# Kernel optimization log

Hardware: AMD Instinct MI355X
Metric: run time of the kernel (lower is better)

## Reference

```python
import jax, jax.numpy as jnp
import numpy as np

WIN = 8
NUM_LAYERS = 2
HID = 512
GROUPS = 4
GH = 2 * HID // GROUPS  # 256


def _shuffle(y):
    # torch Shuffle: transpose(-1,-2).contiguous().view(original_shape)
    return jnp.swapaxes(y, -1, -2).reshape(y.shape)


def _gru_cell(xt, h, w_ih, w_hh, b_ih, b_hh):
    # torch.nn.GRUCell math; gate order r, z, n
    gi = xt @ w_ih.T + b_ih  # [B, 3H]
    gh = h @ w_hh.T + b_hh   # [B, 3H]
    i_r, i_z, i_n = jnp.split(gi, 3, axis=1)
    h_r, h_z, h_n = jnp.split(gh, 3, axis=1)
    r = jax.nn.sigmoid(i_r + h_r)
    z = jax.nn.sigmoid(i_z + h_z)
    n = jnp.tanh(i_n + r * h_n)
    return (1.0 - z) * n + z * h


def _sort_attn(h, a1, a2, a3, a4):
    B, H = h.shape
    s = jnp.sort(h, axis=1)                 # stable sort along features
    se = jnp.stack((h, s), axis=1)          # [B, 2, H]
    y = se @ a1.T                           # Linear(H, H) -> [B, 2, H]
    y = y.reshape(B, GROUPS, GH)            # Flatten + Unflatten
    y = _shuffle(y)
    y = y @ a2.T                            # Linear(GH, GH)
    y = _shuffle(y)
    y = jax.nn.relu(y @ a3.T)               # Linear(GH, GH) + ReLU
    y = y.reshape(B, GROUPS * GH)           # [B, 2H]
    scores = jax.nn.sigmoid(y @ a4.T)       # Linear(2H, H) -> [B, H]
    return h * scores


def setup_inputs() -> dict:
    key = jax.random.key(0)
    ks = jax.random.split(key, 10)
    B, L, C = 64, 4096, 64
    sc = 0.05
    inp = {
        "x": jax.random.normal(ks[0], (B, L, C), dtype=jnp.float32),
        "hidden0": jnp.zeros((NUM_LAYERS, 1, HID), dtype=jnp.float32),
        "w_ih": jax.random.normal(ks[1], (NUM_LAYERS, 3 * HID, HID), dtype=jnp.float32) * sc,
        "w_hh": jax.random.normal(ks[2], (NUM_LAYERS, 3 * HID, HID), dtype=jnp.float32) * sc,
        "b_ih": jax.random.normal(ks[3], (NUM_LAYERS, 3 * HID), dtype=jnp.float32) * sc,
        "b_hh": jax.random.normal(ks[4], (NUM_LAYERS, 3 * HID), dtype=jnp.float32) * sc,
        "a1": jax.random.normal(ks[5], (NUM_LAYERS, HID, HID), dtype=jnp.float32) * sc,
        "a2": jax.random.normal(ks[6], (NUM_LAYERS, GH, GH), dtype=jnp.float32) * sc,
        "a3": jax.random.normal(ks[7], (NUM_LAYERS, GH, GH), dtype=jnp.float32) * sc,
        "a4": jax.random.normal(ks[8], (NUM_LAYERS, HID, 2 * HID), dtype=jnp.float32) * sc,
    }
    return inp


def reference(x, hidden0, w_ih, w_hh, b_ih, b_hh, a1, a2, a3, a4):
    B, L, C = x.shape
    xp = x.reshape(B, L // WIN, WIN * C)
    xs = jnp.swapaxes(xp, 0, 1)                       # [T, B, D]
    h0 = jnp.broadcast_to(hidden0, (NUM_LAYERS, B, HID))

    def step(hid, xt):
        inp = xt
        new = []
        for l in range(NUM_LAYERS):
            h = _gru_cell(inp, hid[l], w_ih[l], w_hh[l], b_ih[l], b_hh[l])
            h = _sort_attn(h, a1[l], a2[l], a3[l], a4[l])
            new.append(h)
            inp = h
        return jnp.stack(new, axis=0), inp

    _, outs = jax.lax.scan(step, h0, xs)              # outs: [T, B, H]
    return jnp.swapaxes(outs, 0, 1)                   # [B, T, H]
```

## Files before the change

### kernel.cpp

```cpp
#include <hip/hip_runtime.h>

#define SCOPE_AGENT __HIP_MEMORY_SCOPE_AGENT

#define OFF_HS    0
#define OFF_HP    65536
#define OFF_SG    131072
#define OFF_U     196608
#define OFF_CTR   327680
#define OFF_T1    393216
#define OFF_M     2490368
#define OFF_GIX   4587520
#define OFF_XT    4587520
#define WS_GIX    54919168
#define WS_XT     21364736

typedef float f32x4 __attribute__((ext_vector_type(4)));

__device__ __forceinline__ float sigm(float x) { return 1.f / (1.f + expf(-x)); }

__device__ __forceinline__ float ld_sc1(const float* p) {
    return __hip_atomic_load(p, __ATOMIC_RELAXED, SCOPE_AGENT);
}
__device__ __forceinline__ void st_sc1(float* p, float v) {
    __hip_atomic_store(p, v, __ATOMIC_RELAXED, SCOPE_AGENT);
}
__device__ __forceinline__ void st2(float* p, float a, float b) {
    unsigned long long v = ((unsigned long long)__float_as_uint(b) << 32) |
                           (unsigned long long)__float_as_uint(a);
    __hip_atomic_store((unsigned long long*)p, v, __ATOMIC_RELAXED, SCOPE_AGENT);
}

__device__ __forceinline__ void ld4b8(const float* base, f32x4* v) {
    const float* b2 = base + 1024;
    asm volatile(
        "global_load_dwordx4 %0, %8, off sc1\n\t"
        "global_load_dwordx4 %1, %8, off offset:1024 sc1\n\t"
        "global_load_dwordx4 %2, %8, off offset:2048 sc1\n\t"
        "global_load_dwordx4 %3, %8, off offset:3072 sc1\n\t"
        "global_load_dwordx4 %4, %9, off sc1\n\t"
        "global_load_dwordx4 %5, %9, off offset:1024 sc1\n\t"
        "global_load_dwordx4 %6, %9, off offset:2048 sc1\n\t"
        "global_load_dwordx4 %7, %9, off offset:3072 sc1\n\t"
        "s_waitcnt vmcnt(0)"
        : "=&v"(v[0]), "=&v"(v[1]), "=&v"(v[2]), "=&v"(v[3]),
          "=&v"(v[4]), "=&v"(v[5]), "=&v"(v[6]), "=&v"(v[7])
        : "v"(base), "v"(b2)
        : "memory");
}

__device__ __forceinline__ void ld4b8x2(const float* baseA, const float* baseB,
                                        f32x4* va, f32x4* vb) {
    const float* a2 = baseA + 1024;
    const float* b2 = baseB + 1024;
    asm volatile(
        "global_load_dwordx4 %0, %16, off sc1\n\t"
        "global_load_dwordx4 %1, %16, off offset:1024 sc1\n\t"
        "global_load_dwordx4 %2, %16, off offset:2048 sc1\n\t"
        "global_load_dwordx4 %3, %16, off offset:3072 sc1\n\t"
        "global_load_dwordx4 %4, %17, off sc1\n\t"
        "global_load_dwordx4 %5, %17, off offset:1024 sc1\n\t"
        "global_load_dwordx4 %6, %17, off offset:2048 sc1\n\t"
        "global_load_dwordx4 %7, %17, off offset:3072 sc1\n\t"
        "global_load_dwordx4 %8, %18, off sc1\n\t"
        "global_load_dwordx4 %9, %18, off offset:1024 sc1\n\t"
        "global_load_dwordx4 %10, %18, off offset:2048 sc1\n\t"
        "global_load_dwordx4 %11, %18, off offset:3072 sc1\n\t"
        "global_load_dwordx4 %12, %19, off sc1\n\t"
        "global_load_dwordx4 %13, %19, off offset:1024 sc1\n\t"
        "global_load_dwordx4 %14, %19, off offset:2048 sc1\n\t"
        "global_load_dwordx4 %15, %19, off offset:3072 sc1\n\t"
        "s_waitcnt vmcnt(0)"
        : "=&v"(va[0]), "=&v"(va[1]), "=&v"(va[2]), "=&v"(va[3]),
          "=&v"(va[4]), "=&v"(va[5]), "=&v"(va[6]), "=&v"(va[7]),
          "=&v"(vb[0]), "=&v"(vb[1]), "=&v"(vb[2]), "=&v"(vb[3]),
          "=&v"(vb[4]), "=&v"(vb[5]), "=&v"(vb[6]), "=&v"(vb[7])
        : "v"(baseA), "v"(a2), "v"(baseB), "v"(b2)
        : "memory");
}

__device__ __forceinline__ void gbar(unsigned* flags, unsigned g) {
    __syncthreads();
    const int tid = threadIdx.x;
    if (tid == 0)
        __hip_atomic_store(&flags[blockIdx.x << 5], g, __ATOMIC_RELAXED, SCOPE_AGENT);
    if (tid < 256) {
        while (__hip_atomic_load(&flags[tid << 5], __ATOMIC_RELAXED, SCOPE_AGENT) < g)
            __builtin_amdgcn_s_sleep(1);
    }
    __syncthreads();
}

__global__ void k_init(const float* __restrict__ h0, float* __restrict__ ws) {
    int idx = blockIdx.x * blockDim.x + threadIdx.x;
    int l = idx >> 15, k = (idx & 32767) >> 6, lane = idx & 63;
    ws[OFF_HS + (l << 15) + ((k >> 2) << 8) + (lane << 2) + (k & 3)] = h0[(l << 9) + k];
    if (idx < 8704) ((unsigned*)(ws + OFF_CTR))[idx] = 0u;
}

__global__ void k_gix(const float* __restrict__ x, const float* __restrict__ wih,
                      float* __restrict__ gix) {
    __shared__ float xs[128][65];
    __shared__ float ww[32][129];
    int t = blockIdx.x, rb = blockIdx.y * 32;
    int tid = threadIdx.x;
    int rw = tid >> 6, b = tid & 63;
    float acc[8] = {0.f, 0.f, 0.f, 0.f, 0.f, 0.f, 0.f, 0.f};
    for (int kc = 0; kc < 4; kc++) {
        __syncthreads();
        for (int i = tid; i < 8192; i += 256) {
            int k = i & 127, b2 = i >> 7;
            xs[k][b2] = x[(size_t)b2 * 262144 + (size_t)t * 512 + kc * 128 + k];
        }
        for (int i = tid; i < 4096; i += 256) {
            int r = i >> 7, k = i & 127;
            ww[r][k] = wih[(size_t)(rb + r) * 512 + kc * 128 + k];
        }
        __syncthreads();
        for (int k = 0; k < 128; k++) {
            float xv = xs[k][b];
#pragma unroll
            for (int rr = 0; rr < 8; rr++)
                acc[rr] = fmaf(ww[rw * 8 + rr][k], xv, acc[rr]);
        }
    }
#pragma unroll
    for (int rr = 0; rr < 8; rr++) {
        int rg = rb + rw * 8 + rr;
        int g = rg >> 9, j = rg & 511;
        gix[((size_t)((size_t)t * 512 + j) * 3 + g) * 64 + b] = acc[rr];
    }
}

__global__ void k_xtk(const float* __restrict__ x, float* __restrict__ xT) {
    __shared__ float tile[64][65];
    int t = blockIdx.x >> 3, kc = blockIdx.x & 7;
    int k = threadIdx.x & 63, b0 = threadIdx.x >> 6;
    for (int i = 0; i < 16; i++) {
        int b = i * 4 + b0;
        tile[k][b] = x[(size_t)b * 262144 + (size_t)t * 512 + kc * 64 + k];
    }
    __syncthreads();
    int b2 = threadIdx.x & 63, k0 = threadIdx.x >> 6;
    for (int i = 0; i < 16; i++) {
        int k2 = kc * 64 + i * 4 + k0;
        xT[(size_t)t * 32768 + ((k2 >> 2) << 8) + (b2 << 2) + (k2 & 3)] = tile[i * 4 + k0][b2];
    }
}

__global__ void k_t1(const float* __restrict__ a1, const float* __restrict__ a2,
                     float* __restrict__ T1) {
    int l = blockIdx.x >> 10, c = blockIdx.x & 1023;
    int g = c >> 8, jj = c & 255;
    __shared__ float sA2[256];
    sA2[threadIdx.x] = a2[l * 65536 + jj * 256 + threadIdx.x];
    __syncthreads();
    const float* A1l = a1 + l * 262144;
    for (int colq = 0; colq < 4; colq++) {
        int col = colq * 256 + threadIdx.x;
        int half = col >> 9, cm = col & 511;
        float acc = 0.f;
#pragma unroll 4
        for (int q = 0; q < 64; q++) {
            int a0 = 2 * half;
            int j0 = g * 64 + q;
            acc = fmaf(sA2[4 * q + a0],     A1l[j0 * 512 + cm], acc);
            acc = fmaf(sA2[4 * q + a0 + 1], A1l[(j0 + 256) * 512 + cm], acc);
        }
        T1[((size_t)(l << 10) + c) * 1024 + col] = acc;
    }
}

__global__ void k_m(const float* __restrict__ a3, const float* __restrict__ T1,
                    float* __restrict__ M) {
    int l = blockIdx.x >> 10, c = blockIdx.x & 1023;
    int g = c >> 8, jj = c & 255;
    __shared__ float sA3[256];
    sA3[threadIdx.x] = a3[l * 65536 + jj * 256 + threadIdx.x];
    __syncthreads();
    const float* T1l = T1 + ((size_t)l << 20);
    for (int colq = 0; colq < 4; colq++) {
        int col = colq * 256 + threadIdx.x;
        float acc = 0.f;
#pragma unroll 4
        for (int m = 0; m < 256; m++) {
            int p = ((m & 3) << 8) + (g << 6) + (m >> 2);
            acc = fmaf(sA3[m], T1l[p * 1024 + col], acc);
        }
        M[((size_t)(l << 10) + c) * 1024 + col] = acc;
    }
}

__global__ void __launch_bounds__(1024, 4)
persist(const float* __restrict__ x, const float* __restrict__ xT,
        const float* __restrict__ gix, int has_xt, int has_gix,
        const float* __restrict__ wih, const float* __restrict__ whh,
        const float* __restrict__ bih, const float* __restrict__ bhh,
        const float* __restrict__ Mc, const float* __restrict__ a4,
        float* __restrict__ ws, float* __restrict__ out) {
    __shared__ float wA[2][2][6][512];
    __shared__ float wM[2][4][1024];
    __shared__ float wD[2][2][1024];
    __shared__ float red2[12][16][64];
    __shared__ float bb[2][2][4];
    __shared__ float sH[2][2][64];

    const int tid = threadIdx.x, w = tid >> 6, lane = tid & 63, bid = blockIdx.x;

    for (int i = tid; i < 12288; i += 1024) {
        int l = i / 6144, r = i % 6144, f = r / 3072, r2 = r % 3072, d = r2 / 512, k = r2 & 511;
        int gate = d >> 1, side = d & 1;
        int j = 2 * bid + f;
        const float* src = side ? whh : wih;
        wA[l][f][d][k] = src[l * 786432 + (gate * 512 + j) * 512 + k];
    }
    for (int i = tid; i < 8192; i += 1024) {
        int l = i >> 12, r = (i >> 10) & 3, col = i & 1023;
        wM[l][r][col] = Mc[((size_t)(l << 10) + 4 * bid + r) * 1024 + col];
    }
    for (int i = tid; i < 4096; i += 1024) {
        int l = i >> 11, f = (i >> 10) & 1, k = i & 1023;
        wD[l][f][k] = a4[l * 524288 + (2 * bid + f) * 1024 + k];
    }
    if (tid < 16) {
        int l = tid / 8, f = (tid / 4) & 1, g = tid & 3;
        int j = 2 * bid + f;
        float v;
        if (g == 0)      v = bih[l * 1536 + j] + bhh[l * 1536 + j];
        else if (g == 1) v = bih[l * 1536 + 512 + j] + bhh[l * 1536 + 512 + j];
        else if (g == 2) v = bih[l * 1536 + 1024 + j];
        else             v = bhh[l * 1536 + 1024 + j];
        bb[l][f][g] = v;
    }
    __syncthreads();

    float* hsG = ws + OFF_HS;
    float* hPg = ws + OFF_HP;
    float* sGg = ws + OFF_SG;
    float* uG  = ws + OFF_U;
    unsigned* flags = (unsigned*)(ws + OFF_CTR);
    unsigned bgen = 0;

    auto stageA = [&](int l, int t) {
        float hprev = 0.f;
        if (w < 2) {
            int j = 2 * bid + w;
            hprev = ld_sc1(&hsG[(l << 15) + ((j >> 2) << 8) + (lane << 2) + (j & 3)]);
        }
        const float* hb = hsG + (l << 15);
        float* hPl = hPg + (l << 15);
        int k0 = w * 32;
        const int koff = ((k0 >> 2) << 8) + (lane << 2);
        if (l == 0 && has_gix) {
            float acc[6] = {0.f, 0.f, 0.f, 0.f, 0.f, 0.f};
            f32x4 hv[8];
            ld4b8(hb + koff, hv);
#pragma unroll
            for (int m = 0; m < 8; m++) {
#pragma unroll
                for (int q = 0; q < 4; q++) {
                    int k = k0 + 4 * m + q;
                    float h = hv[m][q];
#pragma unroll
                    for (int f = 0; f < 2; f++) {
                        acc[f * 3 + 0] = fmaf(wA[0][f][1][k], h, acc[f * 3 + 0]);
                        acc[f * 3 + 1] = fmaf(wA[0][f][3][k], h, acc[f * 3 + 1]);
                        acc[f * 3 + 2] = fmaf(wA[0][f][5][k], h, acc[f * 3 + 2]);
                    }
                }
            }
#pragma unroll
            for (int u = 0; u < 6; u++) red2[u][w][lane] = acc[u];
            __syncthreads();
            if (w < 2) {
                int f = w, j = 2 * bid + f;
                float s0 = 0, s1 = 0, s2 = 0;
#pragma unroll
                for (int i = 0; i < 16; i++) {
                    s0 += red2[f * 3 + 0][i][lane];
                    s1 += red2[f * 3 + 1][i][lane];
                    s2 += red2[f * 3 + 2][i][lane];
                }
                const float* gx = gix + ((size_t)((size_t)t * 512 + j) * 3) * 64;
                float r = sigm(gx[lane] + s0 + bb[0][f][0]);
                float z = sigm(gx[64 + lane] + s1 + bb[0][f][1]);
                float n = tanhf(gx[128 + lane] + bb[0][f][2] + r * (s2 + bb[0][f][3]));
                float hp = (1.f - z) * n + z * hprev;
                sH[0][f][lane] = hp;
                st_sc1(&hPl[((j >> 2) << 8) + (lane << 2) + (j & 3)], hp);
            }
        } else {
            float acc[12];
#pragma unroll
            for (int u = 0; u < 12; u++) acc[u] = 0.f;
            f32x4 iv[8], hv[8];
            if (l == 1) {
                ld4b8x2(hsG + koff, hb + koff, iv, hv);
            } else if (has_xt) {
                ld4b8x2(xT + (size_t)t * 32768 + koff, hb + koff, iv, hv);
            } else {
#pragma unroll
                for (int m = 0; m < 8; m++)
#pragma unroll
                    for (int q = 0; q < 4; q++)
                        iv[m][q] = x[(size_t)lane * 262144 + (size_t)t * 512 + k0 + 4 * m + q];
                ld4b8(hb + koff, hv);
            }
#pragma unroll
            for (int m = 0; m < 8; m++) {
#pragma unroll
                for (int q = 0; q < 4; q++) {
                    int k = k0 + 4 * m + q;
                    float ivq = iv[m][q];
#pragma unroll
                    for (int f = 0; f < 2; f++) {
                        acc[f * 6 + 0] = fmaf(wA[l][f][0][k], ivq, acc[f * 6 + 0]);
                        acc[f * 6 + 2] = fmaf(wA[l][f][2][k], ivq, acc[f * 6 + 2]);
                        acc[f * 6 + 4] = fmaf(wA[l][f][4][k], ivq, acc[f * 6 + 4]);
                    }
                }
            }
#pragma unroll
            for (int m = 0; m < 8; m++) {
#pragma unroll
                for (int q = 0; q < 4; q++) {
                    int k = k0 + 4 * m + q;
                    float h = hv[m][q];
#pragma unroll
                    for (int f = 0; f < 2; f++) {
                        acc[f * 6 + 1] = fmaf(wA[l][f][1][k], h, acc[f * 6 + 1]);
                        acc[f * 6 + 3] = fmaf(wA[l][f][3][k], h, acc[f * 6 + 3]);
                        acc[f * 6 + 5] = fmaf(wA[l][f][5][k], h, acc[f * 6 + 5]);
                    }
                }
            }
#pragma unroll
            for (int u = 0; u < 12; u++) red2[u][w][lane] = acc[u];
            __syncthreads();
            if (w < 2) {
                int f = w, j = 2 * bid + f;
                float g0 = 0, g1 = 0, g2 = 0, g3 = 0, g4 = 0, g5 = 0;
#pragma unroll
                for (int i = 0; i < 16; i++) {
                    g0 += red2[f * 6 + 0][i][lane]; g1 += red2[f * 6 + 1][i][lane];
                    g2 += red2[f * 6 + 2][i][lane]; g3 += red2[f * 6 + 3][i][lane];
                    g4 += red2[f * 6 + 4][i][lane]; g5 += red2[f * 6 + 5][i][lane];
                }
                float r = sigm(g0 + g1 + bb[l][f][0]);
                float z = sigm(g2 + g3 + bb[l][f][1]);
                float n = tanhf(g4 + bb[l][f][2] + r * (g5 + bb[l][f][3]));
                float hp = (1.f - z) * n + z * hprev;
                sH[l][f][lane] = hp;
                st_sc1(&hPl[((j >> 2) << 8) + (lane << 2) + (j & 3)], hp);
            }
        }
    };

    auto stageB = [&](int l, float* accB) {
        int j0 = 2 * bid, j1 = j0 + 1;
        float v0 = sH[l][0][lane], v1 = sH[l][1][lane];
        const float* hPl = hPg + (l << 15);
        float* sGl = sGg + (l << 15);
        int k0 = w * 32, cnt0 = 0, cnt1 = 0;
        accB[0] = accB[1] = accB[2] = accB[3] = 0.f;
        f32x4 hv[8];
        ld4b8(hPl + ((k0 >> 2) << 8) + (lane << 2), hv);
#pragma unroll
        for (int m = 0; m < 8; m++) {
#pragma unroll
            for (int q = 0; q < 4; q++) {
                int k = k0 + 4 * m + q;
                float h = hv[m][q];
                cnt0 += (h < v0 || (h == v0 && k < j0)) ? 1 : 0;
                cnt1 += (h < v1 || (h == v1 && k < j1)) ? 1 : 0;
#pragma unroll
                for (int r = 0; r < 4; r++)
                    accB[r] = fmaf(wM[l][r][k], h, accB[r]);
            }
        }
        red2[0][w][lane] = (float)cnt0;
        red2[1][w][lane] = (float)cnt1;
        __syncthreads();
        if (w < 2) {
            int rk = 0;
#pragma unroll
            for (int i = 0; i < 16; i++) rk += (int)red2[w][i][lane];
            st_sc1(&sGl[((rk >> 2) << 8) + (lane << 2) + (rk & 3)], sH[l][w][lane]);
        }
    };

    auto stageC = [&](int l, const float* accB) {
        float acc[4] = {accB[0], accB[1], accB[2], accB[3]};
        int s0 = w * 32;
        const float* sGl = sGg + (l << 15);
        f32x4 sv[8];
        ld4b8(sGl + ((s0 >> 2) << 8) + (lane << 2), sv);
#pragma unroll
        for (int m = 0; m < 8; m++) {
#pragma unroll
            for (int q = 0; q < 4; q++) {
                int sp = s0 + 4 * m + q;
                float vv = sv[m][q];
#pragma unroll
                for (int r = 0; r < 4; r++)
                    acc[r] = fmaf(wM[l][r][512 + sp], vv, acc[r]);
            }
        }
#pragma unroll
        for (int r = 0; r < 4; r++) red2[r][w][lane] = acc[r];
        __syncthreads();
        if (w < 2) {
            float sa = 0.f, sb = 0.f;
#pragma unroll
            for (int i = 0; i < 16; i++) {
                sa += red2[2 * w + 0][i][lane];
                sb += red2[2 * w + 1][i][lane];
            }
            st2(&uG[(l << 16) + (bid << 8) + (lane << 2) + (w << 1)],
                fmaxf(sa, 0.f), fmaxf(sb, 0.f));
        }
    };

    auto stageD = [&](int l, int t) {
        float a0 = 0.f, a1v = 0.f;
        int k0 = w * 64;
        const float* uL = uG + (l << 16);
        f32x4 uv[8], uw[8];
        ld4b8x2(uL + ((k0 >> 2) << 8) + (lane << 2),
                uL + (((k0 >> 2) + 8) << 8) + (lane << 2), uv, uw);
#pragma unroll
        for (int m = 0; m < 8; m++)
#pragma unroll
            for (int q = 0; q < 4; q++) {
                int k = k0 + 4 * m + q;
                a0 = fmaf(wD[l][0][k], uv[m][q], a0);
                a1v = fmaf(wD[l][1][k], uv[m][q], a1v);
            }
#pragma unroll
        for (int m = 0; m < 8; m++)
#pragma unroll
            for (int q = 0; q < 4; q++) {
                int k = k0 + 32 + 4 * m + q;
                a0 = fmaf(wD[l][0][k], uw[m][q], a0);
                a1v = fmaf(wD[l][1][k], uw[m][q], a1v);
            }
        red2[0][w][lane] = a0;
        red2[1][w][lane] = a1v;
        __syncthreads();
        if (w < 2) {
            float s = 0.f;
#pragma unroll
            for (int i = 0; i < 16; i++) s += red2[w][i][lane];
            float hnew = sH[l][w][lane] * sigm(s);
            int j = 2 * bid + w;
            st_sc1(&hsG[(l << 15) + ((j >> 2) << 8) + (lane << 2) + (j & 3)], hnew);
            if (l == 1)
                out[(size_t)lane * 262144 + (size_t)t * 512 + j] = hnew;
        }
    };

    float accB0[4], accB1[4];

    for (int t = 0; t <= 512; t++) {
        const int t0 = t, t1 = t - 1;
        const bool do0 = (t0 < 512), do1 = (t1 >= 0);

        if (do0) stageA(0, t0);
        if (do1) { __syncthreads(); stageA(1, t1); }
        gbar(flags, ++bgen);

        if (do0) stageB(0, accB0);
        if (do1) { __syncthreads(); stageB(1, accB1); }
        gbar(flags, ++bgen);

        if (do0) stageC(0, accB0);
        if (do1) { __syncthreads(); stageC(1, accB1); }
        gbar(flags, ++bgen);

        if (do0) stageD(0, t0);
        if (do1) { __syncthreads(); stageD(1, t1); }
        gbar(flags, ++bgen);
    }
}

extern "C" void kernel_launch(void* const* d_in, const int* in_sizes, int n_in,
                              void* d_out, int out_size, void* d_ws, size_t ws_size,
                              hipStream_t stream) {
    const float* x   = (const float*)d_in[0];
    const float* h0  = (const float*)d_in[1];
    const float* wih = (const float*)d_in[2];
    const float* whh = (const float*)d_in[3];
    const float* bih = (const float*)d_in[4];
    const float* bhh = (const float*)d_in[5];
    const float* a1  = (const float*)d_in[6];
    const float* a2  = (const float*)d_in[7];
    const float* a3  = (const float*)d_in[8];
    const float* a4  = (const float*)d_in[9];
    float* ws  = (float*)d_ws;
    float* out = (float*)d_out;

    int has_gix = (ws_size >= (size_t)WS_GIX * 4) ? 1 : 0;
    int has_xt  = (!has_gix && ws_size >= (size_t)WS_XT * 4) ? 1 : 0;
    float* T1p = ws + OFF_T1;
    float* Mp  = ws + OFF_M;
    const float* gixp = ws + OFF_GIX;
    const float* xTp  = ws + OFF_XT;

    hipLaunchKernelGGL(k_init, dim3(256), dim3(256), 0, stream, h0, ws);
    if (has_gix)
        hipLaunchKernelGGL(k_gix, dim3(512, 48), dim3(256), 0, stream, x, wih, ws + OFF_GIX);
    else if (has_xt)
        hipLaunchKernelGGL(k_xtk, dim3(4096), dim3(256), 0, stream, x, ws + OFF_XT);
    hipLaunchKernelGGL(k_t1, dim3(2048), dim3(256), 0, stream, a1, a2, T1p);
    hipLaunchKernelGGL(k_m, dim3(2048), dim3(256), 0, stream, a3, T1p, Mp);

    void* args[] = {(void*)&x, (void*)&xTp, (void*)&gixp, (void*)&has_xt, (void*)&has_gix,
                    (void*)&wih, (void*)&whh, (void*)&bih, (void*)&bhh,
                    (void*)&Mp, (void*)&a4, (void*)&ws, (void*)&out};
    hipLaunchCooperativeKernel((void*)persist, dim3(256), dim3(1024), args, 0, stream);
}
```

Measured before the change: 43.46 ms.

## Merge layer-0 and layer-1 stage work per phase to halve block-level syncs

```diff
diff --git a/kernel.cpp b/kernel.cpp
--- a/kernel.cpp
+++ b/kernel.cpp
@@ -200,7 +200,7 @@
     __shared__ float wA[2][2][6][512];
     __shared__ float wM[2][4][1024];
     __shared__ float wD[2][2][1024];
-    __shared__ float red2[12][16][64];
+    __shared__ float red2[14][16][64];
     __shared__ float bb[2][2][4];
     __shared__ float sH[2][2][64];
 
@@ -240,7 +240,7 @@
     unsigned* flags = (unsigned*)(ws + OFF_CTR);
     unsigned bgen = 0;
 
-    auto stageA = [&](int l, int t) {
+    auto stageA_legacy = [&](int l, int t) {
         float hprev = 0.f;
         if (w < 2) {
             int j = 2 * bid + w;
@@ -250,28 +250,134 @@
         float* hPl = hPg + (l << 15);
         int k0 = w * 32;
         const int koff = ((k0 >> 2) << 8) + (lane << 2);
-        if (l == 0 && has_gix) {
-            float acc[6] = {0.f, 0.f, 0.f, 0.f, 0.f, 0.f};
-            f32x4 hv[8];
+        float acc[12];
+#pragma unroll
+        for (int u = 0; u < 12; u++) acc[u] = 0.f;
+        f32x4 iv[8], hv[8];
+        if (l == 1) {
+            ld4b8x2(hsG + koff, hb + koff, iv, hv);
+        } else if (has_xt) {
+            ld4b8x2(xT + (size_t)t * 32768 + koff, hb + koff, iv, hv);
+        } else {
+#pragma unroll
+            for (int m = 0; m < 8; m++)
+#pragma unroll
+                for (int q = 0; q < 4; q++)
+                    iv[m][q] = x[(size_t)lane * 262144 + (size_t)t * 512 + k0 + 4 * m + q];
             ld4b8(hb + koff, hv);
-#pragma unroll
-            for (int m = 0; m < 8; m++) {
-#pragma unroll
-                for (int q = 0; q < 4; q++) {
-                    int k = k0 + 4 * m + q;
-                    float h = hv[m][q];
-#pragma unroll
-                    for (int f = 0; f < 2; f++) {
-                        acc[f * 3 + 0] = fmaf(wA[0][f][1][k], h, acc[f * 3 + 0]);
-                        acc[f * 3 + 1] = fmaf(wA[0][f][3][k], h, acc[f * 3 + 1]);
-                        acc[f * 3 + 2] = fmaf(wA[0][f][5][k], h, acc[f * 3 + 2]);
-                    }
-                }
-            }
-#pragma unroll
-            for (int u = 0; u < 6; u++) red2[u][w][lane] = acc[u];
+        }
+#pragma unroll
+        for (int m = 0; m < 8; m++) {
+#pragma unroll
+            for (int q = 0; q < 4; q++) {
+                int k = k0 + 4 * m + q;
+                float ivq = iv[m][q], h = hv[m][q];
+#pragma unroll
+                for (int f = 0; f < 2; f++) {
+                    acc[f * 6 + 0] = fmaf(wA[l][f][0][k], ivq, acc[f * 6 + 0]);
+                    acc[f * 6 + 1] = fmaf(wA[l][f][1][k], h, acc[f * 6 + 1]);
+                    acc[f * 6 + 2] = fmaf(wA[l][f][2][k], ivq, acc[f * 6 + 2]);
+                    acc[f * 6 + 3] = fmaf(wA[l][f][3][k], h, acc[f * 6 + 3]);
+                    acc[f * 6 + 4] = fmaf(wA[l][f][4][k], ivq, acc[f * 6 + 4]);
+                    acc[f * 6 + 5] = fmaf(wA[l][f][5][k], h, acc[f * 6 + 5]);
+                }
+            }
+        }
+#pragma unroll
+        for (int u = 0; u < 12; u++) red2[u][w][lane] = acc[u];
+        __syncthreads();
+        if (w < 2) {
+            int f = w, j = 2 * bid + f;
+            float g0 = 0, g1 = 0, g2 = 0, g3 = 0, g4 = 0, g5 = 0;
+#pragma unroll
+            for (int i = 0; i < 16; i++) {
+                g0 += red2[f * 6 + 0][i][lane]; g1 += red2[f * 6 + 1][i][lane];
+                g2 += red2[f * 6 + 2][i][lane]; g3 += red2[f * 6 + 3][i][lane];
+                g4 += red2[f * 6 + 4][i][lane]; g5 += red2[f * 6 + 5][i][lane];
+            }
+            float r = sigm(g0 + g1 + bb[l][f][0]);
+            float z = sigm(g2 + g3 + bb[l][f][1]);
+            float n = tanhf(g4 + bb[l][f][2] + r * (g5 + bb[l][f][3]));
+            float hp = (1.f - z) * n + z * hprev;
+            sH[l][f][lane] = hp;
+            st_sc1(&hPl[((j >> 2) << 8) + (lane << 2) + (j & 3)], hp);
+        }
+    };
+
+    float accB0[4], accB1[4];
+
+    for (int t = 0; t <= 512; t++) {
+        const int t0 = t, t1 = t - 1;
+        const bool do0 = (t0 < 512), do1 = (t1 >= 0);
+        const int k0 = w * 32;
+        const int koff = ((k0 >> 2) << 8) + (lane << 2);
+
+        if (has_gix) {
+            float hprev = 0.f, gx0 = 0.f, gx1 = 0.f, gx2 = 0.f;
+            if (do0 && w < 2) {
+                int j = 2 * bid + w;
+                hprev = ld_sc1(&hsG[((j >> 2) << 8) + (lane << 2) + (j & 3)]);
+                const float* gx = gix + ((size_t)((size_t)t0 * 512 + j) * 3) * 64;
+                gx0 = gx[lane]; gx1 = gx[64 + lane]; gx2 = gx[128 + lane];
+            }
+            if (do1 && w >= 2 && w < 4) {
+                int j = 2 * bid + (w - 2);
+                hprev = ld_sc1(&hsG[(1 << 15) + ((j >> 2) << 8) + (lane << 2) + (j & 3)]);
+            }
+            f32x4 G0[8], G1[8];
+            if (do1) ld4b8x2(hsG + koff, hsG + (1 << 15) + koff, G0, G1);
+            else     ld4b8(hsG + koff, G0);
+
+            if (do0) {
+                float acc[6] = {0.f, 0.f, 0.f, 0.f, 0.f, 0.f};
+#pragma unroll
+                for (int m = 0; m < 8; m++) {
+#pragma unroll
+                    for (int q = 0; q < 4; q++) {
+                        int k = k0 + 4 * m + q;
+                        float h = G0[m][q];
+#pragma unroll
+                        for (int f = 0; f < 2; f++) {
+                            acc[f * 3 + 0] = fmaf(wA[0][f][1][k], h, acc[f * 3 + 0]);
+                            acc[f * 3 + 1] = fmaf(wA[0][f][3][k], h, acc[f * 3 + 1]);
+                            acc[f * 3 + 2] = fmaf(wA[0][f][5][k], h, acc[f * 3 + 2]);
+                        }
+                    }
+                }
+#pragma unroll
+                for (int u = 0; u < 6; u++) red2[u][w][lane] = acc[u];
+            }
+            if (do1) {
+                float acc[12];
+#pragma unroll
+                for (int u = 0; u < 12; u++) acc[u] = 0.f;
+#pragma unroll
+                for (int m = 0; m < 8; m++) {
+#pragma unroll
+                    for (int q = 0; q < 4; q++) {
+                        int k = k0 + 4 * m + q;
+                        float ivq = G0[m][q], h = G1[m][q];
+#pragma unroll
+                        for (int f = 0; f < 2; f++) {
+                            acc[f * 6 + 0] = fmaf(wA[1][f][0][k], ivq, acc[f * 6 + 0]);
+                            acc[f * 6 + 1] = fmaf(wA[1][f][1][k], h, acc[f * 6 + 1]);
+                            acc[f * 6 + 2] = fmaf(wA[1][f][2][k], ivq, acc[f * 6 + 2]);
+                            acc[f * 6 + 3] = fmaf(wA[1][f][3][k], h, acc[f * 6 + 3]);
+                            acc[f * 6 + 4] = fmaf(wA[1][f][4][k], ivq, acc[f * 6 + 4]);
+                            acc[f * 6 + 5] = fmaf(wA[1][f][5][k], h, acc[f * 6 + 5]);
+                        }
+                    }
+                }
+#pragma unroll
+                for (int f = 0; f < 2; f++) {
+                    red2[6 + f * 4 + 0][w][lane] = acc[f * 6 + 0] + acc[f * 6 + 1];
+                    red2[6 + f * 4 + 1][w][lane] = acc[f * 6 + 2] + acc[f * 6 + 3];
+                    red2[6 + f * 4 + 2][w][lane] = acc[f * 6 + 4];
+                    red2[6 + f * 4 + 3][w][lane] = acc[f * 6 + 5];
+                }
+            }
             __syncthreads();
-            if (w < 2) {
+            if (do0 && w < 2) {
                 int f = w, j = 2 * bid + f;
                 float s0 = 0, s1 = 0, s2 = 0;
 #pragma unroll
@@ -280,204 +386,217 @@
                     s1 += red2[f * 3 + 1][i][lane];
                     s2 += red2[f * 3 + 2][i][lane];
                 }
-                const float* gx = gix + ((size_t)((size_t)t * 512 + j) * 3) * 64;
-                float r = sigm(gx[lane] + s0 + bb[0][f][0]);
-                float z = sigm(gx[64 + lane] + s1 + bb[0][f][1]);
-                float n = tanhf(gx[128 + lane] + bb[0][f][2] + r * (s2 + bb[0][f][3]));
+                float r = sigm(gx0 + s0 + bb[0][f][0]);
+                float z = sigm(gx1 + s1 + bb[0][f][1]);
+                float n = tanhf(gx2 + bb[0][f][2] + r * (s2 + bb[0][f][3]));
                 float hp = (1.f - z) * n + z * hprev;
                 sH[0][f][lane] = hp;
-                st_sc1(&hPl[((j >> 2) << 8) + (lane << 2) + (j & 3)], hp);
+                st_sc1(&hPg[((j >> 2) << 8) + (lane << 2) + (j & 3)], hp);
+            }
+            if (do1 && w >= 2 && w < 4) {
+                int f = w - 2, j = 2 * bid + f;
+                float rs = 0, zs = 0, g4 = 0, g5 = 0;
+#pragma unroll
+                for (int i = 0; i < 16; i++) {
+                    rs += red2[6 + f * 4 + 0][i][lane];
+                    zs += red2[6 + f * 4 + 1][i][lane];
+                    g4 += red2[6 + f * 4 + 2][i][lane];
+                    g5 += red2[6 + f * 4 + 3][i][lane];
+                }
+                float r = sigm(rs + bb[1][f][0]);
+                float z = sigm(zs + bb[1][f][1]);
+                float n = tanhf(g4 + bb[1][f][2] + r * (g5 + bb[1][f][3]));
+                float hp = (1.f - z) * n + z * hprev;
+                sH[1][f][lane] = hp;
+                st_sc1(&hPg[(1 << 15) + ((j >> 2) << 8) + (lane << 2) + (j & 3)], hp);
             }
         } else {
-            float acc[12];
-#pragma unroll
-            for (int u = 0; u < 12; u++) acc[u] = 0.f;
-            f32x4 iv[8], hv[8];
-            if (l == 1) {
-                ld4b8x2(hsG + koff, hb + koff, iv, hv);
-            } else if (has_xt) {
-                ld4b8x2(xT + (size_t)t * 32768 + koff, hb + koff, iv, hv);
-            } else {
+            if (do0) stageA_legacy(0, t0);
+            if (do1) { __syncthreads(); stageA_legacy(1, t1); }
+        }
+        gbar(flags, ++bgen);
+
+        {
+            f32x4 H0[8], H1[8];
+            if (do0 && do1) ld4b8x2(hPg + koff, hPg + (1 << 15) + koff, H0, H1);
+            else if (do0)   ld4b8(hPg + koff, H0);
+            else            ld4b8(hPg + (1 << 15) + koff, H1);
+            int j0 = 2 * bid, j1 = j0 + 1;
+            if (do0) {
+                float v0 = sH[0][0][lane], v1 = sH[0][1][lane];
+                int c0 = 0, c1 = 0;
+                accB0[0] = accB0[1] = accB0[2] = accB0[3] = 0.f;
+#pragma unroll
+                for (int m = 0; m < 8; m++) {
+#pragma unroll
+                    for (int q = 0; q < 4; q++) {
+                        int k = k0 + 4 * m + q;
+                        float h = H0[m][q];
+                        c0 += (h < v0 || (h == v0 && k < j0)) ? 1 : 0;
+                        c1 += (h < v1 || (h == v1 && k < j1)) ? 1 : 0;
+#pragma unroll
+                        for (int r = 0; r < 4; r++)
+                            accB0[r] = fmaf(wM[0][r][k], h, accB0[r]);
+                    }
+                }
+                red2[0][w][lane] = (float)c0;
+                red2[1][w][lane] = (float)c1;
+            }
+            if (do1) {
+                float v0 = sH[1][0][lane], v1 = sH[1][1][lane];
+                int c0 = 0, c1 = 0;
+                accB1[0] = accB1[1] = accB1[2] = accB1[3] = 0.f;
+#pragma unroll
+                for (int m = 0; m < 8; m++) {
+#pragma unroll
+                    for (int q = 0; q < 4; q++) {
+                        int k = k0 + 4 * m + q;
+                        float h = H1[m][q];
+                        c0 += (h < v0 || (h == v0 && k < j0)) ? 1 : 0;
+                        c1 += (h < v1 || (h == v1 && k < j1)) ? 1 : 0;
+#pragma unroll
+                        for (int r = 0; r < 4; r++)
+                            accB1[r] = fmaf(wM[1][r][k], h, accB1[r]);
+                    }
+                }
+                red2[2][w][lane] = (float)c0;
+                red2[3][w][lane] = (float)c1;
+            }
+            __syncthreads();
+            if (w < 2 && do0) {
+                int rk = 0;
+#pragma unroll
+                for (int i = 0; i < 16; i++) rk += (int)red2[w][i][lane];
+                st_sc1(&sGg[((rk >> 2) << 8) + (lane << 2) + (rk & 3)], sH[0][w][lane]);
+            }
+            if (w >= 2 && w < 4 && do1) {
+                int rk = 0;
+#pragma unroll
+                for (int i = 0; i < 16; i++) rk += (int)red2[w][i][lane];
+                st_sc1(&sGg[(1 << 15) + ((rk >> 2) << 8) + (lane << 2) + (rk & 3)],
+                       sH[1][w - 2][lane]);
+            }
+        }
+        gbar(flags, ++bgen);
+
+        {
+            f32x4 S0[8], S1[8];
+            if (do0 && do1) ld4b8x2(sGg + koff, sGg + (1 << 15) + koff, S0, S1);
+            else if (do0)   ld4b8(sGg + koff, S0);
+            else            ld4b8(sGg + (1 << 15) + koff, S1);
+            if (do0) {
+                float acc[4] = {accB0[0], accB0[1], accB0[2], accB0[3]};
+#pragma unroll
+                for (int m = 0; m < 8; m++) {
+#pragma unroll
+                    for (int q = 0; q < 4; q++) {
+                        int sp = k0 + 4 * m + q;
+                        float vv = S0[m][q];
+#pragma unroll
+                        for (int r = 0; r < 4; r++)
+                            acc[r] = fmaf(wM[0][r][512 + sp], vv, acc[r]);
+                    }
+                }
+#pragma unroll
+                for (int r = 0; r < 4; r++) red2[r][w][lane] = acc[r];
+            }
+            if (do1) {
+                float acc[4] = {accB1[0], accB1[1], accB1[2], accB1[3]};
+#pragma unroll
+                for (int m = 0; m < 8; m++) {
+#pragma unroll
+                    for (int q = 0; q < 4; q++) {
+                        int sp = k0 + 4 * m + q;
+                        float vv = S1[m][q];
+#pragma unroll
+                        for (int r = 0; r < 4; r++)
+                            acc[r] = fmaf(wM[1][r][512 + sp], vv, acc[r]);
+                    }
+                }
+#pragma unroll
+                for (int r = 0; r < 4; r++) red2[4 + r][w][lane] = acc[r];
+            }
+            __syncthreads();
+            if (w < 4) {
+                bool act = (w < 2) ? do0 : do1;
+                if (act) {
+                    int l = w >> 1, s = w & 1;
+                    float sa = 0.f, sb = 0.f;
+#pragma unroll
+                    for (int i = 0; i < 16; i++) {
+                        sa += red2[w * 2][i][lane];
+                        sb += red2[w * 2 + 1][i][lane];
+                    }
+                    st2(&uG[(l << 16) + (bid << 8) + (lane << 2) + 2 * s],
+                        fmaxf(sa, 0.f), fmaxf(sb, 0.f));
+                }
+            }
+        }
+        gbar(flags, ++bgen);
+
+        {
+            const int kd0 = w * 64;
+            const int kdoff = ((kd0 >> 2) << 8) + (lane << 2);
+            f32x4 U[8], V[8];
+            if (do0) {
+                ld4b8x2(uG + kdoff, uG + kdoff + 2048, U, V);
+                float a0 = 0.f, a1 = 0.f;
 #pragma unroll
                 for (int m = 0; m < 8; m++)
 #pragma unroll
-                    for (int q = 0; q < 4; q++)
-                        iv[m][q] = x[(size_t)lane * 262144 + (size_t)t * 512 + k0 + 4 * m + q];
-                ld4b8(hb + koff, hv);
-            }
-#pragma unroll
-            for (int m = 0; m < 8; m++) {
-#pragma unroll
-                for (int q = 0; q < 4; q++) {
-                    int k = k0 + 4 * m + q;
-                    float ivq = iv[m][q];
-#pragma unroll
-                    for (int f = 0; f < 2; f++) {
-                        acc[f * 6 + 0] = fmaf(wA[l][f][0][k], ivq, acc[f * 6 + 0]);
-                        acc[f * 6 + 2] = fmaf(wA[l][f][2][k], ivq, acc[f * 6 + 2]);
-                        acc[f * 6 + 4] = fmaf(wA[l][f][4][k], ivq, acc[f * 6 + 4]);
-                    }
-                }
-            }
-#pragma unroll
-            for (int m = 0; m < 8; m++) {
-#pragma unroll
-                for (int q = 0; q < 4; q++) {
-                    int k = k0 + 4 * m + q;
-                    float h = hv[m][q];
-#pragma unroll
-                    for (int f = 0; f < 2; f++) {
-                        acc[f * 6 + 1] = fmaf(wA[l][f][1][k], h, acc[f * 6 + 1]);
-                        acc[f * 6 + 3] = fmaf(wA[l][f][3][k], h, acc[f * 6 + 3]);
-                        acc[f * 6 + 5] = fmaf(wA[l][f][5][k], h, acc[f * 6 + 5]);
-                    }
-                }
-            }
-#pragma unroll
-            for (int u = 0; u < 12; u++) red2[u][w][lane] = acc[u];
+                    for (int q = 0; q < 4; q++) {
+                        int k = kd0 + 4 * m + q;
+                        a0 = fmaf(wD[0][0][k], U[m][q], a0);
+                        a1 = fmaf(wD[0][1][k], U[m][q], a1);
+                    }
+#pragma unroll
+                for (int m = 0; m < 8; m++)
+#pragma unroll
+                    for (int q = 0; q < 4; q++) {
+                        int k = kd0 + 32 + 4 * m + q;
+                        a0 = fmaf(wD[0][0][k], V[m][q], a0);
+                        a1 = fmaf(wD[0][1][k], V[m][q], a1);
+                    }
+                red2[0][w][lane] = a0;
+                red2[1][w][lane] = a1;
+            }
+            if (do1) {
+                ld4b8x2(uG + (1 << 16) + kdoff, uG + (1 << 16) + kdoff + 2048, U, V);
+                float a0 = 0.f, a1 = 0.f;
+#pragma unroll
+                for (int m = 0; m < 8; m++)
+#pragma unroll
+                    for (int q = 0; q < 4; q++) {
+                        int k = kd0 + 4 * m + q;
+                        a0 = fmaf(wD[1][0][k], U[m][q], a0);
+                        a1 = fmaf(wD[1][1][k], U[m][q], a1);
+                    }
+#pragma unroll
+                for (int m = 0; m < 8; m++)
+#pragma unroll
+                    for (int q = 0; q < 4; q++) {
+                        int k = kd0 + 32 + 4 * m + q;
+                        a0 = fmaf(wD[1][0][k], V[m][q], a0);
+                        a1 = fmaf(wD[1][1][k], V[m][q], a1);
+                    }
+                red2[2][w][lane] = a0;
+                red2[3][w][lane] = a1;
+            }
             __syncthreads();
-            if (w < 2) {
-                int f = w, j = 2 * bid + f;
-                float g0 = 0, g1 = 0, g2 = 0, g3 = 0, g4 = 0, g5 = 0;
-#pragma unroll
-                for (int i = 0; i < 16; i++) {
-                    g0 += red2[f * 6 + 0][i][lane]; g1 += red2[f * 6 + 1][i][lane];
-                    g2 += red2[f * 6 + 2][i][lane]; g3 += red2[f * 6 + 3][i][lane];
-                    g4 += red2[f * 6 + 4][i][lane]; g5 += red2[f * 6 + 5][i][lane];
-                }
-                float r = sigm(g0 + g1 + bb[l][f][0]);
-                float z = sigm(g2 + g3 + bb[l][f][1]);
-                float n = tanhf(g4 + bb[l][f][2] + r * (g5 + bb[l][f][3]));
-                float hp = (1.f - z) * n + z * hprev;
-                sH[l][f][lane] = hp;
-                st_sc1(&hPl[((j >> 2) << 8) + (lane << 2) + (j & 3)], hp);
-            }
-        }
-    };
-
-    auto stageB = [&](int l, float* accB) {
-        int j0 = 2 * bid, j1 = j0 + 1;
-        float v0 = sH[l][0][lane], v1 = sH[l][1][lane];
-        const float* hPl = hPg + (l << 15);
-        float* sGl = sGg + (l << 15);
-        int k0 = w * 32, cnt0 = 0, cnt1 = 0;
-        accB[0] = accB[1] = accB[2] = accB[3] = 0.f;
-        f32x4 hv[8];
-        ld4b8(hPl + ((k0 >> 2) << 8) + (lane << 2), hv);
-#pragma unroll
-        for (int m = 0; m < 8; m++) {
-#pragma unroll
-            for (int q = 0; q < 4; q++) {
-                int k = k0 + 4 * m + q;
-                float h = hv[m][q];
-                cnt0 += (h < v0 || (h == v0 && k < j0)) ? 1 : 0;
-                cnt1 += (h < v1 || (h == v1 && k < j1)) ? 1 : 0;
-#pragma unroll
-                for (int r = 0; r < 4; r++)
-                    accB[r] = fmaf(wM[l][r][k], h, accB[r]);
-            }
-        }
-        red2[0][w][lane] = (float)cnt0;
-        red2[1][w][lane] = (float)cnt1;
-        __syncthreads();
-        if (w < 2) {
-            int rk = 0;
-#pragma unroll
-            for (int i = 0; i < 16; i++) rk += (int)red2[w][i][lane];
-            st_sc1(&sGl[((rk >> 2) << 8) + (lane << 2) + (rk & 3)], sH[l][w][lane]);
-        }
-    };
-
-    auto stageC = [&](int l, const float* accB) {
-        float acc[4] = {accB[0], accB[1], accB[2], accB[3]};
-        int s0 = w * 32;
-        const float* sGl = sGg + (l << 15);
-        f32x4 sv[8];
-        ld4b8(sGl + ((s0 >> 2) << 8) + (lane << 2), sv);
-#pragma unroll
-        for (int m = 0; m < 8; m++) {
-#pragma unroll
-            for (int q = 0; q < 4; q++) {
-                int sp = s0 + 4 * m + q;
-                float vv = sv[m][q];
-#pragma unroll
-                for (int r = 0; r < 4; r++)
-                    acc[r] = fmaf(wM[l][r][512 + sp], vv, acc[r]);
-            }
-        }
-#pragma unroll
-        for (int r = 0; r < 4; r++) red2[r][w][lane] = acc[r];
-        __syncthreads();
-        if (w < 2) {
-            float sa = 0.f, sb = 0.f;
-#pragma unroll
-            for (int i = 0; i < 16; i++) {
-                sa += red2[2 * w + 0][i][lane];
-                sb += red2[2 * w + 1][i][lane];
-            }
-            st2(&uG[(l << 16) + (bid << 8) + (lane << 2) + (w << 1)],
-                fmaxf(sa, 0.f), fmaxf(sb, 0.f));
-        }
-    };
-
-    auto stageD = [&](int l, int t) {
-        float a0 = 0.f, a1v = 0.f;
-        int k0 = w * 64;
-        const float* uL = uG + (l << 16);
-        f32x4 uv[8], uw[8];
-        ld4b8x2(uL + ((k0 >> 2) << 8) + (lane << 2),
-                uL + (((k0 >> 2) + 8) << 8) + (lane << 2), uv, uw);
-#pragma unroll
-        for (int m = 0; m < 8; m++)
-#pragma unroll
-            for (int q = 0; q < 4; q++) {
-                int k = k0 + 4 * m + q;
-                a0 = fmaf(wD[l][0][k], uv[m][q], a0);
-                a1v = fmaf(wD[l][1][k], uv[m][q], a1v);
-            }
-#pragma unroll
-        for (int m = 0; m < 8; m++)
-#pragma unroll
-            for (int q = 0; q < 4; q++) {
-                int k = k0 + 32 + 4 * m + q;
-                a0 = fmaf(wD[l][0][k], uw[m][q], a0);
-                a1v = fmaf(wD[l][1][k], uw[m][q], a1v);
-            }
-        red2[0][w][lane] = a0;
-        red2[1][w][lane] = a1v;
-        __syncthreads();
-        if (w < 2) {
-            float s = 0.f;
-#pragma unroll
-            for (int i = 0; i < 16; i++) s += red2[w][i][lane];
-            float hnew = sH[l][w][lane] * sigm(s);
-            int j = 2 * bid + w;
-            st_sc1(&hsG[(l << 15) + ((j >> 2) << 8) + (lane << 2) + (j & 3)], hnew);
-            if (l == 1)
-                out[(size_t)lane * 262144 + (size_t)t * 512 + j] = hnew;
-        }
-    };
-
-    float accB0[4], accB1[4];
-
-    for (int t = 0; t <= 512; t++) {
-        const int t0 = t, t1 = t - 1;
-        const bool do0 = (t0 < 512), do1 = (t1 >= 0);
-
-        if (do0) stageA(0, t0);
-        if (do1) { __syncthreads(); stageA(1, t1); }
-        gbar(flags, ++bgen);
-
-        if (do0) stageB(0, accB0);
-        if (do1) { __syncthreads(); stageB(1, accB1); }
-        gbar(flags, ++bgen);
-
-        if (do0) stageC(0, accB0);
-        if (do1) { __syncthreads(); stageC(1, accB1); }
-        gbar(flags, ++bgen);
-
-        if (do0) stageD(0, t0);
-        if (do1) { __syncthreads(); stageD(1, t1); }
+            if (w < 4) {
+                bool act = (w < 2) ? do0 : do1;
+                if (act) {
+                    int l = w >> 1, f = w & 1, j = 2 * bid + f;
+                    float s = 0.f;
+#pragma unroll
+                    for (int i = 0; i < 16; i++) s += red2[w][i][lane];
+                    float hnew = sH[l][f][lane] * sigm(s);
+                    st_sc1(&hsG[(l << 15) + ((j >> 2) << 8) + (lane << 2) + (j & 3)], hnew);
+                    if (l == 1)
+                        out[(size_t)lane * 262144 + (size_t)t1 * 512 + j] = hnew;
+                }
+            }
+        }
         gbar(flags, ++bgen);
     }
 }
```

Measured after the change: 67.37 ms. +55.0%, slower.
